# Optimization experiments

Measured on AMD Instinct MI355X. Metric: run time of the kernel, lower is better.

## Reference

```python
import jax, jax.numpy as jnp
import numpy as np

N = 50000       # nodes
E = 800000      # edges (avg degree 16)
R = 8           # relations
IN = 128        # in_channels
H = 128         # hidden_size
B = 10          # graphs in batch
NPG = N // B    # nodes per graph (equal-size graphs)
NEG_SLOPE = 0.2 # RGATConv default negative_slope


def setup_inputs() -> dict:
    key = jax.random.key(0)
    ks = jax.random.split(key, 12)
    s = 0.1
    x = jax.random.normal(ks[0], (N, IN), dtype=jnp.float32)
    edge_index = jax.random.randint(ks[1], (2, E), 0, N, dtype=jnp.int32)
    edge_type = jax.random.randint(ks[2], (E,), 0, R, dtype=jnp.int32)
    batch = jnp.repeat(jnp.arange(B, dtype=jnp.int32), NPG)
    W1 = jax.random.normal(ks[3], (R, IN, H), dtype=jnp.float32) * s
    q1 = jax.random.normal(ks[4], (H, 1), dtype=jnp.float32) * s
    k1 = jax.random.normal(ks[5], (H, 1), dtype=jnp.float32) * s
    b1 = jnp.zeros((H,), dtype=jnp.float32)
    W2 = jax.random.normal(ks[6], (R, H, H), dtype=jnp.float32) * s
    q2 = jax.random.normal(ks[7], (H, 1), dtype=jnp.float32) * s
    k2 = jax.random.normal(ks[8], (H, 1), dtype=jnp.float32) * s
    b2 = jnp.zeros((H,), dtype=jnp.float32)
    Wl = jax.random.normal(ks[9], (H, H), dtype=jnp.float32) * s
    bl = jnp.zeros((H,), dtype=jnp.float32)
    return dict(x=x, edge_index=edge_index, edge_type=edge_type, batch=batch,
                W1=W1, q1=q1, k1=k1, b1=b1, W2=W2, q2=q2, k2=k2, b2=b2,
                Wl=Wl, bl=bl)


def _rgat_conv(x, src, tgt, etype, W, q, k, b):
    # Per-relation transform once per node ([R,N,H]), then gather per edge;
    # mathematically identical to PyG's per-edge bmm but avoids the [E,in,H] blowup.
    xW = jnp.einsum('ni,rio->rno', x, W)          # [R, N, H]
    outi = xW[etype, tgt]                          # [E, H] transformed target feats
    outj = xW[etype, src]                          # [E, H] transformed source feats
    # additive self-attention, heads=1, dim=1
    alpha = jax.nn.leaky_relu(outi @ q + outj @ k, NEG_SLOPE)  # [E, 1]
    # across-relation segment softmax over incoming edges of each target node
    m = jax.ops.segment_max(alpha, tgt, num_segments=N)        # [N, 1]
    a = jnp.exp(alpha - m[tgt])
    den = jax.ops.segment_sum(a, tgt, num_segments=N)          # [N, 1]
    a = a / (den[tgt] + 1e-16)
    out = jax.ops.segment_sum(a * outj, tgt, num_segments=N)   # [N, H]
    return out + b


def reference(x, edge_index, edge_type, batch, W1, q1, k1, b1,
              W2, q2, k2, b2, Wl, bl):
    src, tgt = edge_index[0], edge_index[1]
    h = jax.nn.relu(_rgat_conv(x, src, tgt, edge_type, W1, q1, k1, b1))
    # dropout p=0 -> identity
    h = jax.nn.relu(_rgat_conv(h, src, tgt, edge_type, W2, q2, k2, b2))
    h = h @ Wl.T + bl                               # nn.Linear
    # to_dense_batch: batch is sorted with equal-size graphs of NPG nodes
    return h.reshape(B, NPG, H)
```

## Files before the change

kernel.cpp:

```cpp
#include <hip/hip_runtime.h>


typedef unsigned int uint;
typedef unsigned short ushort_t;

using bf16x8 = __attribute__((ext_vector_type(8))) __bf16;
using f32x4  = __attribute__((ext_vector_type(4))) float;

__device__ __forceinline__ ushort_t fToBf(float f) {
  uint u = __float_as_uint(f);
  u += 0x7FFFu + ((u >> 16) & 1);
  return (ushort_t)(u >> 16);
}
__device__ __forceinline__ float bfToF(ushort_t h) {
  return __uint_as_float(((uint)h) << 16);
}
__device__ __forceinline__ uint packBf(float a, float b) {
  return (uint)fToBf(a) | ((uint)fToBf(b) << 16);
}


__global__ void k_count(const int* __restrict__ tgt, int* __restrict__ deg, int E) {
  int e = blockIdx.x * 256 + threadIdx.x;
  if (e < E) atomicAdd(&deg[tgt[e]], 1);
}

__global__ void k_scanA(const int* __restrict__ deg, int* __restrict__ incl,
                        int* __restrict__ bsum, int n) {
  __shared__ int s[256];
  int tid = threadIdx.x;
  int i = blockIdx.x * 256 + tid;
  int v = (i < n) ? deg[i] : 0;
  s[tid] = v;
  __syncthreads();
  for (int off = 1; off < 256; off <<= 1) {
    int t = (tid >= off) ? s[tid - off] : 0;
    __syncthreads();
    s[tid] += t;
    __syncthreads();
  }
  if (i < n) incl[i] = s[tid];
  if (tid == 255) bsum[blockIdx.x] = s[255];
}

__global__ void k_scanB(int* __restrict__ bsum, int nb) {
  __shared__ int s[256];
  int tid = threadIdx.x;
  int v = (tid < nb) ? bsum[tid] : 0;
  s[tid] = v;
  __syncthreads();
  for (int off = 1; off < 256; off <<= 1) {
    int t = (tid >= off) ? s[tid - off] : 0;
    __syncthreads();
    s[tid] += t;
    __syncthreads();
  }
  if (tid < nb) bsum[tid] = s[tid] - v;
}

__global__ void k_scanC(const int* __restrict__ deg, const int* __restrict__ incl,
                        const int* __restrict__ bsum, int* __restrict__ rowptr,
                        int n, int E) {
  int i = blockIdx.x * 256 + threadIdx.x;
  if (i < n) {
    rowptr[i] = bsum[blockIdx.x] + incl[i] - deg[i];
    if (i == n - 1) rowptr[n] = E;
  }
}

__global__ void k_scatter(const int* __restrict__ src, const int* __restrict__ tgt,
                          const int* __restrict__ et, const int* __restrict__ rowptr,
                          int* __restrict__ cursor, int* __restrict__ sorted, int E) {
  int e = blockIdx.x * 256 + threadIdx.x;
  if (e >= E) return;
  int t = tgt[e];
  int pos = atomicAdd(&cursor[t], 1);
  sorted[rowptr[t] + pos] = src[e] | (et[e] << 16);
}


__global__ void k_wTf(const float* __restrict__ W1, const float* __restrict__ W2,
                      ushort_t* __restrict__ WTf) {
  int b = blockIdx.x * 4 + (threadIdx.x >> 6);
  int lane = threadIdx.x & 63;
  int layer = b >> 8;
  int r = (b >> 5) & 7;
  int f = b & 31;
  int mt = f >> 2, kb = f & 3;
  const float* W = layer ? W2 : W1;
  int col = mt * 16 + (lane & 15);
  int krow = kb * 32 + (lane >> 4) * 8;
  ushort_t* dst = WTf + ((size_t)b * 64 + lane) * 8;
  #pragma unroll
  for (int j = 0; j < 8; j++)
    dst[j] = fToBf(W[((size_t)r * 128 + krow + j) * 128 + col]);
}

__global__ void k_wqwk(const float* __restrict__ W1, const float* __restrict__ q1,
                       const float* __restrict__ k1, const float* __restrict__ W2,
                       const float* __restrict__ q2, const float* __restrict__ k2,
                       ushort_t* __restrict__ wqk) {
  int g = blockIdx.x * 256 + threadIdx.x;
  if (g >= 4096) return;
  int layer = g >> 11;
  int which = (g >> 10) & 1;
  int idx = g & 1023;
  const float* w = (layer ? W2 : W1) + (size_t)idx * 128;
  const float* v = layer ? (which ? k2 : q2) : (which ? k1 : q1);
  float s = 0.f;
  #pragma unroll 8
  for (int h = 0; h < 128; h++) s += w[h] * v[h];
  int r = idx >> 7, kin = idx & 127;
  wqk[(size_t)layer * 2048 + ((which << 3) + r) * 128 + kin] = fToBf(s);
}


template <bool F32IN>
__global__ __launch_bounds__(256, 2) void
k_xw(const void* __restrict__ Ain,
     const ushort_t* __restrict__ WTf,
     const ushort_t* __restrict__ Wqk,
     ushort_t* __restrict__ xW,
     float* __restrict__ stbl,
     int M) {
  __shared__ __align__(16) ushort_t wbuf[2][16384];
  int tid = threadIdx.x, wv = tid >> 6, lane = tid & 63;
  int l15 = lane & 15, quad = lane >> 4;
  int node0 = blockIdx.x * 128 + wv * 32;

  bf16x8 bx[2][4];
  #pragma unroll
  for (int tile = 0; tile < 2; tile++) {
    int node = node0 + tile * 16 + l15;
    int nc = node < M ? node : M - 1;
    if (F32IN) {
      const float* row = (const float*)Ain + (size_t)nc * 128;
      #pragma unroll
      for (int kb = 0; kb < 4; kb++) {
        float4 a = *(const float4*)(row + kb * 32 + quad * 8);
        float4 b = *(const float4*)(row + kb * 32 + quad * 8 + 4);
        union { bf16x8 v; ushort_t u[8]; } t;
        t.u[0] = fToBf(a.x); t.u[1] = fToBf(a.y); t.u[2] = fToBf(a.z); t.u[3] = fToBf(a.w);
        t.u[4] = fToBf(b.x); t.u[5] = fToBf(b.y); t.u[6] = fToBf(b.z); t.u[7] = fToBf(b.w);
        bx[tile][kb] = t.v;
      }
    } else {
      const ushort_t* row = (const ushort_t*)Ain + (size_t)nc * 128;
      #pragma unroll
      for (int kb = 0; kb < 4; kb++)
        bx[tile][kb] = *(const bf16x8*)(row + kb * 32 + quad * 8);
    }
  }

  #pragma unroll
  for (int i = 0; i < 8; i++)
    *(int4*)(wbuf[0] + (size_t)(tid + i * 256) * 8) =
        *(const int4*)(WTf + (size_t)(tid + i * 256) * 8);
  __syncthreads();

  for (int r = 0; r < 8; r++) {
    int4 pf[8];
    if (r < 7) {
      const ushort_t* src = WTf + (size_t)(r + 1) * 16384;
      #pragma unroll
      for (int i = 0; i < 8; i++)
        pf[i] = *(const int4*)(src + (size_t)(tid + i * 256) * 8);
    }
    const ushort_t* wb = wbuf[r & 1];
    uint2 po[2][8];
    #pragma unroll
    for (int mt = 0; mt < 8; mt++) {
      f32x4 a0 = {}, a1 = {};
      #pragma unroll
      for (int kb = 0; kb < 4; kb++) {
        bf16x8 af = *(const bf16x8*)(wb + (size_t)((mt * 4 + kb) * 64 + lane) * 8);
        a0 = __builtin_amdgcn_mfma_f32_16x16x32_bf16(af, bx[0][kb], a0, 0, 0, 0);
        a1 = __builtin_amdgcn_mfma_f32_16x16x32_bf16(af, bx[1][kb], a1, 0, 0, 0);
      }
      po[0][mt].x = packBf(a0[0], a0[1]); po[0][mt].y = packBf(a0[2], a0[3]);
      po[1][mt].x = packBf(a1[0], a1[1]); po[1][mt].y = packBf(a1[2], a1[3]);
    }
    #pragma unroll
    for (int tile = 0; tile < 2; tile++) {
      int node = node0 + tile * 16 + l15;
      if (node < M) {
        ushort_t* rowp = xW + ((size_t)r * M + node) * 128 + quad * 32;
        #pragma unroll
        for (int i = 0; i < 4; i++) {
          int4 v = {(int)po[tile][2 * i].x, (int)po[tile][2 * i].y,
                    (int)po[tile][2 * i + 1].x, (int)po[tile][2 * i + 1].y};
          *(int4*)(rowp + i * 8) = v;
        }
      }
    }
    if (r < 7) {
      ushort_t* db = wbuf[(r + 1) & 1];
      #pragma unroll
      for (int i = 0; i < 8; i++)
        *(int4*)(db + (size_t)(tid + i * 256) * 8) = pf[i];
    }
    __syncthreads();
  }

  bf16x8 aq[4];
  #pragma unroll
  for (int kb = 0; kb < 4; kb++)
    aq[kb] = *(const bf16x8*)(Wqk + (size_t)l15 * 128 + kb * 32 + quad * 8);
  #pragma unroll
  for (int tile = 0; tile < 2; tile++) {
    f32x4 s = {};
    #pragma unroll
    for (int kb = 0; kb < 4; kb++)
      s = __builtin_amdgcn_mfma_f32_16x16x32_bf16(aq[kb], bx[tile][kb], s, 0, 0, 0);
    int node = node0 + tile * 16 + l15;
    if (node < M) {
      float4 v = {s[0], s[1], s[2], s[3]};
      *(float4*)(stbl + (size_t)node * 16 + quad * 4) = v;
    }
  }
}


#define ACC8(W_, V_)                                                     \
  acc[0] += W_ * bfToF((ushort_t)(V_.x & 0xFFFF));                       \
  acc[1] += W_ * bfToF((ushort_t)(V_.x >> 16));                          \
  acc[2] += W_ * bfToF((ushort_t)(V_.y & 0xFFFF));                       \
  acc[3] += W_ * bfToF((ushort_t)(V_.y >> 16));                          \
  acc[4] += W_ * bfToF((ushort_t)(V_.z & 0xFFFF));                       \
  acc[5] += W_ * bfToF((ushort_t)(V_.z >> 16));                          \
  acc[6] += W_ * bfToF((ushort_t)(V_.w & 0xFFFF));                       \
  acc[7] += W_ * bfToF((ushort_t)(V_.w >> 16));

__global__ __launch_bounds__(256) void
k_aggr(const ushort_t* __restrict__ feat,
       const float* __restrict__ stbl,
       const int* __restrict__ rowptr, const int* __restrict__ sorted,
       const float* __restrict__ bias, ushort_t* __restrict__ outp, int n) {
  int tid = threadIdx.x, wv = tid >> 6, lane = tid & 63;
  int t = blockIdx.x * 4 + wv;
  if (t >= n) return;
  int e0 = rowptr[t], e1 = rowptr[t + 1];
  int g4 = lane >> 4, fcol = lane & 15;

  float m = -INFINITY, den = 0.f;
  float acc[8] = {};

  for (int base = e0; base < e1; base += 64) {
    int cnt = min(64, e1 - base);
    float alpha = -INFINITY;
    int pk = 0;
    if (lane < cnt) {
      pk = sorted[base + lane];
      int s = pk & 0xFFFF, r = pk >> 16;
      float a = stbl[(size_t)t * 16 + r] + stbl[(size_t)s * 16 + 8 + r];
      alpha = (a >= 0.f) ? a : 0.2f * a;
    }
    float cm = alpha;
    #pragma unroll
    for (int off = 32; off; off >>= 1) cm = fmaxf(cm, __shfl_xor(cm, off, 64));
    float nm = fmaxf(m, cm);
    float sc = __expf(m - nm);
    den *= sc;
    #pragma unroll
    for (int i = 0; i < 8; i++) acc[i] *= sc;
    float w = (lane < cnt) ? __expf(alpha - nm) : 0.f;
    float ws = w;
    #pragma unroll
    for (int off = 32; off; off >>= 1) ws += __shfl_xor(ws, off, 64);
    den += ws;
    m = nm;

    for (int g = 0; g < cnt; g += 16) {
      int i0 = g + g4;
      float w0 = __shfl(w, i0, 64);
      float w1 = __shfl(w, i0 + 4, 64);
      float w2 = __shfl(w, i0 + 8, 64);
      float w3 = __shfl(w, i0 + 12, 64);
      int p0 = __shfl(pk, i0, 64);
      int p1 = __shfl(pk, i0 + 4, 64);
      int p2 = __shfl(pk, i0 + 8, 64);
      int p3 = __shfl(pk, i0 + 12, 64);
      const uint4* r0 = (const uint4*)(feat + (size_t)((p0 >> 16) * n + (p0 & 0xFFFF)) * 128) + fcol;
      const uint4* r1 = (const uint4*)(feat + (size_t)((p1 >> 16) * n + (p1 & 0xFFFF)) * 128) + fcol;
      const uint4* r2 = (const uint4*)(feat + (size_t)((p2 >> 16) * n + (p2 & 0xFFFF)) * 128) + fcol;
      const uint4* r3 = (const uint4*)(feat + (size_t)((p3 >> 16) * n + (p3 & 0xFFFF)) * 128) + fcol;
      uint4 v0 = *r0;
      uint4 v1 = *r1;
      uint4 v2 = *r2;
      uint4 v3 = *r3;
      ACC8(w0, v0)
      ACC8(w1, v1)
      ACC8(w2, v2)
      ACC8(w3, v3)
    }
  }

  #pragma unroll
  for (int i = 0; i < 8; i++) acc[i] += __shfl_xor(acc[i], 16, 64);
  #pragma unroll
  for (int i = 0; i < 8; i++) acc[i] += __shfl_xor(acc[i], 32, 64);

  float inv = (den > 0.f) ? 1.f / (den + 1e-16f) : 0.f;
  int base0 = (fcol & 3) * 32 + (fcol >> 2) * 4;
  float4 ba = *(const float4*)(bias + base0);
  float4 bb = *(const float4*)(bias + base0 + 16);
  uint2 oa, ob;
  oa.x = packBf(fmaxf(acc[0] * inv + ba.x, 0.f), fmaxf(acc[1] * inv + ba.y, 0.f));
  oa.y = packBf(fmaxf(acc[2] * inv + ba.z, 0.f), fmaxf(acc[3] * inv + ba.w, 0.f));
  ob.x = packBf(fmaxf(acc[4] * inv + bb.x, 0.f), fmaxf(acc[5] * inv + bb.y, 0.f));
  ob.y = packBf(fmaxf(acc[6] * inv + bb.z, 0.f), fmaxf(acc[7] * inv + bb.w, 0.f));
  if (lane < 16) {
    *(uint2*)(outp + (size_t)t * 128 + base0) = oa;
    *(uint2*)(outp + (size_t)t * 128 + base0 + 16) = ob;
  }
}


#define LDA 136

__global__ __launch_bounds__(256) void
k_gemmL(const ushort_t* __restrict__ A, const float* __restrict__ Wl,
        float* __restrict__ Cout, const float* __restrict__ bias, int M) {
  __shared__ ushort_t As[64 * LDA];
  __shared__ ushort_t Bs[128 * LDA];
  int tid = threadIdx.x;
  int row0 = blockIdx.x * 64;
  for (int c = tid; c < 1024; c += 256) {
    int r = c >> 4, off = (c & 15) * 8;
    int4 v = {0, 0, 0, 0};
    if (row0 + r < M) v = *(const int4*)(A + (size_t)(row0 + r) * 128 + off);
    *(int4*)(As + r * LDA + off) = v;
  }
  for (int c = tid; c < 2048; c += 256) {
    int nn = c >> 4, off = (c & 15) * 8;
    float4 a = *(const float4*)(Wl + (size_t)nn * 128 + off);
    float4 b = *(const float4*)(Wl + (size_t)nn * 128 + off + 4);
    ushort_t* d = Bs + nn * LDA + off;
    d[0] = fToBf(a.x); d[1] = fToBf(a.y); d[2] = fToBf(a.z); d[3] = fToBf(a.w);
    d[4] = fToBf(b.x); d[5] = fToBf(b.y); d[6] = fToBf(b.z); d[7] = fToBf(b.w);
  }
  __syncthreads();
  int wv = tid >> 6, lane = tid & 63;
  int l15 = lane & 15, quad = lane >> 4;
  int wr = wv * 16;
  bf16x8 afr[4];
  #pragma unroll
  for (int kb = 0; kb < 4; kb++)
    afr[kb] = *reinterpret_cast<const bf16x8*>(As + (wr + l15) * LDA + kb * 32 + quad * 8);
  f32x4 acc[8] = {};
  #pragma unroll
  for (int ct = 0; ct < 8; ct++)
    #pragma unroll
    for (int kb = 0; kb < 4; kb++) {
      bf16x8 bfr = *reinterpret_cast<const bf16x8*>(Bs + (ct * 16 + l15) * LDA + kb * 32 + quad * 8);
      acc[ct] = __builtin_amdgcn_mfma_f32_16x16x32_bf16(afr[kb], bfr, acc[ct], 0, 0, 0);
    }
  #pragma unroll
  for (int ct = 0; ct < 8; ct++)
    #pragma unroll
    for (int reg = 0; reg < 4; reg++) {
      int rr = row0 + wr + quad * 4 + reg;
      if (rr < M) Cout[(size_t)rr * 128 + ct * 16 + l15] = acc[ct][reg] + bias[ct * 16 + l15];
    }
}


extern "C" void kernel_launch(void* const* d_in, const int* in_sizes, int n_in,
                              void* d_out, int out_size, void* d_ws, size_t ws_size,
                              hipStream_t stream) {
  const float* x   = (const float*)d_in[0];
  const int* ei    = (const int*)d_in[1];
  const int* etype = (const int*)d_in[2];
  const float* W1  = (const float*)d_in[4];
  const float* q1  = (const float*)d_in[5];
  const float* k1  = (const float*)d_in[6];
  const float* b1  = (const float*)d_in[7];
  const float* W2  = (const float*)d_in[8];
  const float* q2  = (const float*)d_in[9];
  const float* k2  = (const float*)d_in[10];
  const float* b2  = (const float*)d_in[11];
  const float* Wl  = (const float*)d_in[12];
  const float* bl  = (const float*)d_in[13];
  float* out       = (float*)d_out;

  const int N = in_sizes[0] / 128;
  const int E = in_sizes[2];

  char* ws = (char*)d_ws;
  size_t off = 0;
  auto alloc = [&](size_t bytes) {
    size_t o = off;
    off = (off + bytes + 255) & ~(size_t)255;
    return o;
  };

  ushort_t* xW    = (ushort_t*)(ws + alloc((size_t)8 * N * 128 * 2));
  ushort_t* h1    = (ushort_t*)(ws + alloc((size_t)N * 128 * 2));
  ushort_t* h2    = (ushort_t*)(ws + alloc((size_t)N * 128 * 2));
  ushort_t* WTf   = (ushort_t*)(ws + alloc((size_t)2 * 8 * 16384 * 2));
  ushort_t* wqk   = (ushort_t*)(ws + alloc(2 * 16 * 128 * 2));
  float* stblA    = (float*)(ws + alloc((size_t)N * 16 * 4));
  float* stblB    = (float*)(ws + alloc((size_t)N * 16 * 4));
  int* deg        = (int*)(ws + alloc((size_t)N * 4));
  int* cursor     = (int*)(ws + alloc((size_t)N * 4));
  int* incl       = (int*)(ws + alloc((size_t)N * 4));
  int* rowptr     = (int*)(ws + alloc((size_t)(N + 1) * 4));
  int* bsum       = (int*)(ws + alloc(256 * 4));
  int* sorted     = (int*)(ws + alloc((size_t)E * 4));
  (void)ws_size; (void)n_in; (void)out_size;

  const int* srcp = ei;
  const int* tgtp = ei + E;

  int gE = (E + 255) / 256;
  int gN = (N + 255) / 256;
  int gW = (N + 3) / 4;
  int gX = (N + 127) / 128;
  int gL = (N + 63) / 64;

  hipMemsetAsync(deg, 0, (size_t)N * 4, stream);
  hipMemsetAsync(cursor, 0, (size_t)N * 4, stream);
  k_count<<<gE, 256, 0, stream>>>(tgtp, deg, E);
  k_scanA<<<gN, 256, 0, stream>>>(deg, incl, bsum, N);
  k_scanB<<<1, 256, 0, stream>>>(bsum, gN);
  k_scanC<<<gN, 256, 0, stream>>>(deg, incl, bsum, rowptr, N, E);
  k_scatter<<<gE, 256, 0, stream>>>(srcp, tgtp, etype, rowptr, cursor, sorted, E);

  k_wTf<<<128, 256, 0, stream>>>(W1, W2, WTf);
  k_wqwk<<<16, 256, 0, stream>>>(W1, q1, k1, W2, q2, k2, wqk);

  k_xw<true><<<gX, 256, 0, stream>>>(x, WTf, wqk, xW, stblA, N);
  k_aggr<<<gW, 256, 0, stream>>>(xW, stblA, rowptr, sorted, b1, h1, N);

  k_xw<false><<<gX, 256, 0, stream>>>(h1, WTf + (size_t)8 * 16384,
                                      wqk + 2048, xW, stblB, N);
  k_aggr<<<gW, 256, 0, stream>>>(xW, stblB, rowptr, sorted, b2, h2, N);

  k_gemmL<<<gL, 256, 0, stream>>>(h2, Wl, out, bl, N);
}
```

Baseline: 396.8 us.

## Split per-node transform kernel across relations via second grid dimension

The k_xw kernel previously looped over all 8 relations in one block, double-buffering each relation's weight tile through shared memory. It now launches one block per (node tile, relation) pair, loads a single relation's weights into a halved shared buffer, and raises the launch-bounds occupancy hint from 2 to 4 blocks per unit. The goal is more parallelism and occupancy and the removal of the serial per-relation sync and prefetch chain. In exchange, each input row is reloaded, and converted from f32 when needed, 8 times. The attention-score table is still computed only by the relation-0 blocks.

```diff
diff --git a/kernel.cpp b/kernel.cpp
--- a/kernel.cpp
+++ b/kernel.cpp
@@ -116,17 +116,26 @@
 
 
 template <bool F32IN>
-__global__ __launch_bounds__(256, 2) void
+__global__ __launch_bounds__(256, 4) void
 k_xw(const void* __restrict__ Ain,
      const ushort_t* __restrict__ WTf,
      const ushort_t* __restrict__ Wqk,
      ushort_t* __restrict__ xW,
      float* __restrict__ stbl,
      int M) {
-  __shared__ __align__(16) ushort_t wbuf[2][16384];
+  __shared__ __align__(16) ushort_t wbuf[16384];
   int tid = threadIdx.x, wv = tid >> 6, lane = tid & 63;
   int l15 = lane & 15, quad = lane >> 4;
+  int r = blockIdx.y;
   int node0 = blockIdx.x * 128 + wv * 32;
+
+  {
+    const ushort_t* src = WTf + (size_t)r * 16384;
+    #pragma unroll
+    for (int i = 0; i < 8; i++)
+      *(int4*)(wbuf + (size_t)(tid + i * 256) * 8) =
+          *(const int4*)(src + (size_t)(tid + i * 256) * 8);
+  }
 
   bf16x8 bx[2][4];
   #pragma unroll
@@ -152,70 +161,51 @@
     }
   }
 
-  #pragma unroll
-  for (int i = 0; i < 8; i++)
-    *(int4*)(wbuf[0] + (size_t)(tid + i * 256) * 8) =
-        *(const int4*)(WTf + (size_t)(tid + i * 256) * 8);
   __syncthreads();
 
-  for (int r = 0; r < 8; r++) {
-    int4 pf[8];
-    if (r < 7) {
-      const ushort_t* src = WTf + (size_t)(r + 1) * 16384;
+  uint2 po[2][8];
+  #pragma unroll
+  for (int mt = 0; mt < 8; mt++) {
+    f32x4 a0 = {}, a1 = {};
+    #pragma unroll
+    for (int kb = 0; kb < 4; kb++) {
+      bf16x8 af = *(const bf16x8*)(wbuf + (size_t)((mt * 4 + kb) * 64 + lane) * 8);
+      a0 = __builtin_amdgcn_mfma_f32_16x16x32_bf16(af, bx[0][kb], a0, 0, 0, 0);
+      a1 = __builtin_amdgcn_mfma_f32_16x16x32_bf16(af, bx[1][kb], a1, 0, 0, 0);
+    }
+    po[0][mt].x = packBf(a0[0], a0[1]); po[0][mt].y = packBf(a0[2], a0[3]);
+    po[1][mt].x = packBf(a1[0], a1[1]); po[1][mt].y = packBf(a1[2], a1[3]);
+  }
+  #pragma unroll
+  for (int tile = 0; tile < 2; tile++) {
+    int node = node0 + tile * 16 + l15;
+    if (node < M) {
+      ushort_t* rowp = xW + ((size_t)r * M + node) * 128 + quad * 32;
       #pragma unroll
-      for (int i = 0; i < 8; i++)
-        pf[i] = *(const int4*)(src + (size_t)(tid + i * 256) * 8);
-    }
-    const ushort_t* wb = wbuf[r & 1];
-    uint2 po[2][8];
-    #pragma unroll
-    for (int mt = 0; mt < 8; mt++) {
-      f32x4 a0 = {}, a1 = {};
+      for (int i = 0; i < 4; i++) {
+        int4 v = {(int)po[tile][2 * i].x, (int)po[tile][2 * i].y,
+                  (int)po[tile][2 * i + 1].x, (int)po[tile][2 * i + 1].y};
+        *(int4*)(rowp + i * 8) = v;
+      }
+    }
+  }
+
+  if (r == 0) {
+    bf16x8 aq[4];
+    #pragma unroll
+    for (int kb = 0; kb < 4; kb++)
+      aq[kb] = *(const bf16x8*)(Wqk + (size_t)l15 * 128 + kb * 32 + quad * 8);
+    #pragma unroll
+    for (int tile = 0; tile < 2; tile++) {
+      f32x4 s = {};
       #pragma unroll
-      for (int kb = 0; kb < 4; kb++) {
-        bf16x8 af = *(const bf16x8*)(wb + (size_t)((mt * 4 + kb) * 64 + lane) * 8);
-        a0 = __builtin_amdgcn_mfma_f32_16x16x32_bf16(af, bx[0][kb], a0, 0, 0, 0);
-        a1 = __builtin_amdgcn_mfma_f32_16x16x32_bf16(af, bx[1][kb], a1, 0, 0, 0);
-      }
-      po[0][mt].x = packBf(a0[0], a0[1]); po[0][mt].y = packBf(a0[2], a0[3]);
-      po[1][mt].x = packBf(a1[0], a1[1]); po[1][mt].y = packBf(a1[2], a1[3]);
-    }
-    #pragma unroll
-    for (int tile = 0; tile < 2; tile++) {
+      for (int kb = 0; kb < 4; kb++)
+        s = __builtin_amdgcn_mfma_f32_16x16x32_bf16(aq[kb], bx[tile][kb], s, 0, 0, 0);
       int node = node0 + tile * 16 + l15;
       if (node < M) {
-        ushort_t* rowp = xW + ((size_t)r * M + node) * 128 + quad * 32;
-        #pragma unroll
-        for (int i = 0; i < 4; i++) {
-          int4 v = {(int)po[tile][2 * i].x, (int)po[tile][2 * i].y,
-                    (int)po[tile][2 * i + 1].x, (int)po[tile][2 * i + 1].y};
-          *(int4*)(rowp + i * 8) = v;
-        }
+        float4 v = {s[0], s[1], s[2], s[3]};
+        *(float4*)(stbl + (size_t)node * 16 + quad * 4) = v;
       }
-    }
-    if (r < 7) {
-      ushort_t* db = wbuf[(r + 1) & 1];
-      #pragma unroll
-      for (int i = 0; i < 8; i++)
-        *(int4*)(db + (size_t)(tid + i * 256) * 8) = pf[i];
-    }
-    __syncthreads();
-  }
-
-  bf16x8 aq[4];
-  #pragma unroll
-  for (int kb = 0; kb < 4; kb++)
-    aq[kb] = *(const bf16x8*)(Wqk + (size_t)l15 * 128 + kb * 32 + quad * 8);
-  #pragma unroll
-  for (int tile = 0; tile < 2; tile++) {
-    f32x4 s = {};
-    #pragma unroll
-    for (int kb = 0; kb < 4; kb++)
-      s = __builtin_amdgcn_mfma_f32_16x16x32_bf16(aq[kb], bx[tile][kb], s, 0, 0, 0);
-    int node = node0 + tile * 16 + l15;
-    if (node < M) {
-      float4 v = {s[0], s[1], s[2], s[3]};
-      *(float4*)(stbl + (size_t)node * 16 + quad * 4) = v;
     }
   }
 }
@@ -415,7 +405,7 @@
   int gE = (E + 255) / 256;
   int gN = (N + 255) / 256;
   int gW = (N + 3) / 4;
-  int gX = (N + 127) / 128;
+  int NB = (N + 127) / 128;
   int gL = (N + 63) / 64;
 
   hipMemsetAsync(deg, 0, (size_t)N * 4, stream);
@@ -429,11 +419,11 @@
   k_wTf<<<128, 256, 0, stream>>>(W1, W2, WTf);
   k_wqwk<<<16, 256, 0, stream>>>(W1, q1, k1, W2, q2, k2, wqk);
 
-  k_xw<true><<<gX, 256, 0, stream>>>(x, WTf, wqk, xW, stblA, N);
+  k_xw<true><<<dim3(NB, 8), 256, 0, stream>>>(x, WTf, wqk, xW, stblA, N);
   k_aggr<<<gW, 256, 0, stream>>>(xW, stblA, rowptr, sorted, b1, h1, N);
 
-  k_xw<false><<<gX, 256, 0, stream>>>(h1, WTf + (size_t)8 * 16384,
-                                      wqk + 2048, xW, stblB, N);
+  k_xw<false><<<dim3(NB, 8), 256, 0, stream>>>(h1, WTf + (size_t)8 * 16384,
+                                               wqk + 2048, xW, stblB, N);
   k_aggr<<<gW, 256, 0, stream>>>(xW, stblB, rowptr, sorted, b2, h2, N);
 
   k_gemmL<<<gL, 256, 0, stream>>>(h2, Wl, out, bl, N);
```

Measured after the change: 412.0 us. 1.04x slower.
